# Performance work log

Hardware: AMD Instinct MI355X
Metric: run time of the kernel (lower is better)

## Reference

```python
import jax, jax.numpy as jnp
import numpy as np

DIM = 1024
H = 8            # heads (light and heavy)
DH = 64          # dim_head
W = 64           # local attention window (light_window_size // 2)
NQ = 512         # num_heavy_tokens_q
NKV = 1024       # num_heavy_tokens_kv
EPS = 1.0        # coor descent eps
NITERS = 50      # coor descent iters
FETCH = 9.0 / 8.0
SCALE = DH ** -0.5


def _ln(x, w, b):
    m = x.mean(-1, keepdims=True)
    v = ((x - m) ** 2).mean(-1, keepdims=True)
    return (x - m) * jax.lax.rsqrt(v + 1e-5) * w + b


def _rms(x, g):
    n = jnp.maximum(jnp.linalg.norm(x, axis=-1, keepdims=True), 1e-12)
    return x / n * np.sqrt(DIM).astype(np.float32) * g


def local_attn(x, Wqkv, Wout):
    # LocalMHA, non-causal, look_backward=1, look_forward=1, window W
    b, n, _ = x.shape
    nw = n // W
    qkv = x @ Wqkv.T                      # [b,n,3*H*DH]
    q, k, v = jnp.split(qkv, 3, axis=-1)
    def towin(t):
        return t.reshape(b, nw, W, H, DH).transpose(0, 3, 1, 2, 4)  # [b,h,nw,w,dh]
    q, k, v = map(towin, (q, k, v))
    def expand(t):  # gather prev/cur/next windows -> [b,h,nw,3w,dh]
        tp = jnp.pad(t, ((0, 0), (0, 0), (1, 1), (0, 0), (0, 0)))
        return jnp.concatenate([tp[:, :, :-2], tp[:, :, 1:-1], tp[:, :, 2:]], axis=3)
    ke, ve = expand(k), expand(v)
    sim = jnp.einsum('bhnid,bhnjd->bhnij', q, ke) * SCALE
    win = jnp.arange(nw)
    valid = jnp.concatenate([
        jnp.repeat((win > 0)[:, None], W, 1),
        jnp.ones((nw, W), bool),
        jnp.repeat((win < nw - 1)[:, None], W, 1)], axis=1)  # [nw,3w]
    sim = jnp.where(valid[None, None, :, None, :], sim, -1e9)
    attn = jax.nn.softmax(sim, axis=-1)
    o = jnp.einsum('bhnij,bhnjd->bhnid', attn, ve)
    o = o.transpose(0, 2, 3, 1, 4).reshape(b, n, H * DH)
    return o @ Wout.T


def route(x, routing_token, num_tokens):
    # CoordinateDescentRouter with num_routing_tokens=1, straight_through=True
    s = jnp.einsum('bnd,rd->brn', x, routing_token).reshape(x.shape[0], x.shape[1])
    n = s.shape[-1]
    logk = jnp.log(jnp.asarray(min(num_tokens * FETCH, float(n)), s.dtype))
    def body(ab, _):
        a, bb = ab
        a = EPS * (logk - jax.nn.logsumexp((s + bb) / EPS, axis=-1, keepdims=True))
        bb = -jax.nn.relu(s + a)
        return (a, bb), None
    (a, bb), _ = jax.lax.scan(body, (jnp.zeros((s.shape[0], 1), s.dtype), -s), None, length=NITERS)
    scores = jnp.exp((s + a + bb) / EPS)
    sel_scores, sel_idx = jax.lax.top_k(scores, num_tokens)
    # straight-through: forward value 1.0, gradient of identity
    sel_scores = sel_scores + jax.lax.stop_gradient(1.0 - sel_scores)
    return sel_scores, sel_idx


def heavy_attn(xq, ctx, scores_kv, gamma, Wq, Wkv, Wout, null_kv):
    b = xq.shape[0]
    xq = _rms(xq, gamma)
    ctx = _rms(ctx, gamma)
    q = (xq @ Wq.T).reshape(b, -1, H, DH).transpose(0, 2, 1, 3)           # [b,h,nq,dh]
    kv = (ctx @ Wkv.T).reshape(b, -1, H, 2 * DH).transpose(0, 2, 1, 3)    # [b,h,nkv,2dh]
    k, v = kv[..., :DH], kv[..., DH:]
    v = v * scores_kv[:, None, :, None]
    nk = jnp.broadcast_to(null_kv[0][None, :, None, :], (b, H, 1, DH))
    nv = jnp.broadcast_to(null_kv[1][None, :, None, :], (b, H, 1, DH))
    k = jnp.concatenate([nk, k], axis=2)
    v = jnp.concatenate([nv, v], axis=2)
    sim = jnp.einsum('bhid,bhjd->bhij', q, k) * SCALE
    attn = jax.nn.softmax(sim, axis=-1)
    o = jnp.einsum('bhij,bhjd->bhid', attn, v)
    o = o.transpose(0, 2, 1, 3).reshape(b, -1, H * DH)
    return o @ Wout.T


def setup_inputs() -> dict:
    key = jax.random.key(0)
    ks = jax.random.split(key, 12)
    D, IN = DIM, H * DH
    w = lambda k, shape: jax.random.normal(k, shape, jnp.float32) * 0.02
    return {
        'x': jax.random.normal(ks[0], (4, 4096, D), jnp.float32),
        'ln_w': jnp.ones((D,), jnp.float32),
        'ln_b': jnp.zeros((D,), jnp.float32),
        'Wqkv': w(ks[1], (3 * IN, D)),
        'Wout_l': w(ks[2], (D, IN)),
        'rt_q': jax.random.normal(ks[3], (1, D), jnp.float32),
        'rt_kv': jax.random.normal(ks[4], (1, D), jnp.float32),
        'gamma': jnp.ones((D,), jnp.float32),
        'Wq': w(ks[5], (IN, D)),
        'Wkv': w(ks[6], (2 * IN, D)),
        'Wout_h': w(ks[7], (D, IN)),
        'null_kv': jax.random.normal(ks[8], (2, H, DH), jnp.float32),
        'null_q': jax.random.normal(ks[9], (D,), jnp.float32),
    }


def reference(x, ln_w, ln_b, Wqkv, Wout_l, rt_q, rt_kv, gamma, Wq, Wkv, Wout_h, null_kv, null_q):
    b, n, d = x.shape
    light = local_attn(_ln(x, ln_w, ln_b), Wqkv, Wout_l)
    sq, iq = route(x, rt_q, NQ)
    skv, ikv = route(x, rt_kv, NKV)
    br = jnp.arange(b)[:, None]
    xq = x[br, iq]          # gather routed queries  [b,NQ,d]
    xkv = x[br, ikv]        # gather routed kv       [b,NKV,d]
    heavy = heavy_attn(xq, xkv, skv, gamma, Wq, Wkv, Wout_h, null_kv)
    heavy = heavy * sq[..., None]
    out = jnp.broadcast_to(null_q[None, None, :], (b, n, d))
    out = out.at[br, iq].set(heavy)   # scatter heavy branch back
    return out + light
```

## Files before the change

kernel.cpp:

```cpp
#include <hip/hip_runtime.h>
#include <hip/hip_bf16.h>

typedef __attribute__((ext_vector_type(8))) short bv8;
typedef __attribute__((ext_vector_type(4))) float fv4;
typedef __hip_bfloat16 bf16;

#define MFMA16(a,b,c) __builtin_amdgcn_mfma_f32_16x16x32_bf16((a),(b),(c),0,0,0)
#define GLOAD_LDS(gp, lp) __builtin_amdgcn_global_load_lds( \
    (const __attribute__((address_space(1))) void*)(gp), \
    (__attribute__((address_space(3))) void*)(lp), 16, 0, 0)

template<int NW>
__device__ __forceinline__ float blockReduceSumF(float v) {
  #pragma unroll
  for (int m = 1; m < 64; m <<= 1) v += __shfl_xor(v, m, 64);
  __shared__ float sm[NW];
  if ((threadIdx.x & 63) == 0) sm[threadIdx.x >> 6] = v;
  __syncthreads();
  float t = 0.f;
  #pragma unroll
  for (int i = 0; i < NW; ++i) t += sm[i];
  __syncthreads();
  return t;
}

template<int NW>
__device__ __forceinline__ double blockReduceMaxD(double v) {
  #pragma unroll
  for (int m = 1; m < 64; m <<= 1) v = fmax(v, __shfl_xor(v, m, 64));
  __shared__ double sm[NW];
  if ((threadIdx.x & 63) == 0) sm[threadIdx.x >> 6] = v;
  __syncthreads();
  double t = sm[0];
  #pragma unroll
  for (int i = 1; i < NW; ++i) t = fmax(t, sm[i]);
  __syncthreads();
  return t;
}

__global__ __launch_bounds__(256)
void prep_kernel(const float* __restrict__ x, const float* __restrict__ lnw,
                 const float* __restrict__ lnb, const float* __restrict__ rtq,
                 const float* __restrict__ rtkv, bf16* __restrict__ lnout,
                 double* __restrict__ s,
                 const float* __restrict__ a0, const float* __restrict__ a1,
                 const float* __restrict__ a2, const float* __restrict__ a3,
                 const float* __restrict__ a4,
                 bf16* __restrict__ b0, bf16* __restrict__ b1, bf16* __restrict__ b2,
                 bf16* __restrict__ b3, bf16* __restrict__ b4,
                 int* __restrict__ posq) {
  const int bid = blockIdx.x;
  if (bid < 16384) {
    const int r = bid;
    const float* xr = x + (size_t)r * 1024;
    float v4[4]; float ssum = 0.f;
    double dq = 0.0, dk = 0.0;
    #pragma unroll
    for (int i = 0; i < 4; ++i) {
      int d = threadIdx.x + i * 256;
      float v = xr[d];
      v4[i] = v; ssum += v;
      dq += (double)v * (double)rtq[d];
      dk += (double)v * (double)rtkv[d];
    }
    ssum = blockReduceSumF<4>(ssum);
    const float mean = ssum * (1.0f / 1024.0f);
    float vs = 0.f;
    #pragma unroll
    for (int i = 0; i < 4; ++i) { float d = v4[i] - mean; vs += d * d; }
    vs = blockReduceSumF<4>(vs);
    const float rstd = 1.0f / sqrtf(vs * (1.0f / 1024.0f) + 1e-5f);
    #pragma unroll
    for (int m = 1; m < 64; m <<= 1) { dq += __shfl_xor(dq, m, 64); dk += __shfl_xor(dk, m, 64); }
    __shared__ double smq[4], smk[4];
    if ((threadIdx.x & 63) == 0) { smq[threadIdx.x >> 6] = dq; smk[threadIdx.x >> 6] = dk; }
    __syncthreads();
    if (threadIdx.x == 0) {
      s[r] = smq[0] + smq[1] + smq[2] + smq[3];
      s[16384 + r] = smk[0] + smk[1] + smk[2] + smk[3];
    }
    bf16* orow = lnout + (size_t)r * 1024;
    #pragma unroll
    for (int i = 0; i < 4; ++i) {
      int d = threadIdx.x + i * 256;
      orow[d] = __float2bfloat16((v4[i] - mean) * rstd * lnw[d] + lnb[d]);
    }
  } else if (bid < 18432) {
    size_t g = ((size_t)(bid - 16384) * 256 + threadIdx.x) * 8;
    const float* src; bf16* dst; size_t off;
    if (g < 1572864)      { src = a0; dst = b0; off = g; }
    else if (g < 2097152) { src = a1; dst = b1; off = g - 1572864; }
    else if (g < 2621440) { src = a2; dst = b2; off = g - 2097152; }
    else if (g < 3670016) { src = a3; dst = b3; off = g - 2621440; }
    else                  { src = a4; dst = b4; off = g - 3670016; }
    float4 v0 = *(const float4*)(src + off);
    float4 v1 = *(const float4*)(src + off + 4);
    bv8 o;
    ((bf16*)&o)[0] = __float2bfloat16(v0.x); ((bf16*)&o)[1] = __float2bfloat16(v0.y);
    ((bf16*)&o)[2] = __float2bfloat16(v0.z); ((bf16*)&o)[3] = __float2bfloat16(v0.w);
    ((bf16*)&o)[4] = __float2bfloat16(v1.x); ((bf16*)&o)[5] = __float2bfloat16(v1.y);
    ((bf16*)&o)[6] = __float2bfloat16(v1.z); ((bf16*)&o)[7] = __float2bfloat16(v1.w);
    *(bv8*)(dst + off) = o;
  } else {
    int i0 = (bid - 18432) * 1024 + threadIdx.x * 4;
    posq[i0] = -1; posq[i0 + 1] = -1; posq[i0 + 2] = -1; posq[i0 + 3] = -1;
  }
}

template<int EPI>
__device__ __forceinline__ void gemm_core(
    const bf16* __restrict__ A, const bf16* __restrict__ B, void* __restrict__ Cout,
    int N, int K, int row0, int col0, bf16* As, bf16* Bs,
    const int* __restrict__ posq, const float* __restrict__ heavy,
    const float* __restrict__ nullq) {
  const int tid = threadIdx.x;
  const int lane = tid & 63, w = tid >> 6;
  const int wr = w >> 1, wc = w & 1;
  const int lrow = lane & 15, lkg = lane >> 4;
  fv4 acc[4][4];
  #pragma unroll
  for (int m = 0; m < 4; ++m)
    #pragma unroll
    for (int n = 0; n < 4; ++n) acc[m][n] = (fv4){0.f, 0.f, 0.f, 0.f};
  const int ob0 = w * 1024;
  for (int k0 = 0; k0 < K; k0 += 64) {
    #pragma unroll
    for (int t = 0; t < 4; ++t) {
      int ob = t * 4096 + ob0;
      int byteL = ob + lane * 16;
      int r = byteL >> 7;
      int cU = ((byteL >> 4) & 7) ^ (r & 7);
      GLOAD_LDS(A + (size_t)(row0 + r) * K + k0 + cU * 8, (char*)As + ob);
      GLOAD_LDS(B + (size_t)(col0 + r) * K + k0 + cU * 8, (char*)Bs + ob);
    }
    __syncthreads();
    #pragma unroll
    for (int ks = 0; ks < 2; ++ks) {
      bv8 af[4], bfr[4];
      #pragma unroll
      for (int m = 0; m < 4; ++m) {
        int row = wr * 64 + m * 16 + lrow;
        af[m] = *(bv8*)((char*)As + row * 128 + (((ks * 4 + lkg) ^ (row & 7)) << 4));
      }
      #pragma unroll
      for (int n = 0; n < 4; ++n) {
        int row = wc * 64 + n * 16 + lrow;
        bfr[n] = *(bv8*)((char*)Bs + row * 128 + (((ks * 4 + lkg) ^ (row & 7)) << 4));
      }
      #pragma unroll
      for (int m = 0; m < 4; ++m)
        #pragma unroll
        for (int n = 0; n < 4; ++n)
          acc[m][n] = MFMA16(af[m], bfr[n], acc[m][n]);
    }
    __syncthreads();
  }
  #pragma unroll
  for (int m = 0; m < 4; ++m) {
    int gr0 = row0 + wr * 64 + m * 16 + (lane >> 4) * 4;
    #pragma unroll
    for (int n = 0; n < 4; ++n) {
      int gc = col0 + wc * 64 + n * 16 + lrow;
      #pragma unroll
      for (int r = 0; r < 4; ++r) {
        int grow = gr0 + r;
        float vv = acc[m][n][r];
        if (EPI == 0) {
          ((bf16*)Cout)[(size_t)grow * N + gc] = __float2bfloat16(vv);
        } else if (EPI == 1) {
          ((float*)Cout)[(size_t)grow * N + gc] = vv;
        } else {
          int p = posq[grow];
          float add = (p >= 0) ? heavy[((size_t)((grow >> 12) * 512 + p)) * 1024 + gc]
                               : nullq[gc];
          ((float*)Cout)[(size_t)grow * N + gc] = vv + add;
        }
      }
    }
  }
}

__device__ __forceinline__ void xcd_remap(int d, int gx, int& row0, int& col0) {
  int q = d >> 3;
  col0 = (q % gx) * 128;
  row0 = ((d & 7) + 8 * (q / gx)) * 128;
}

template<int EPI>
__global__ __launch_bounds__(256)
void gemm_bt(const bf16* __restrict__ A, const bf16* __restrict__ B, void* __restrict__ Cout,
             int N, int K,
             const int* __restrict__ posq, const float* __restrict__ heavy,
             const float* __restrict__ nullq) {
  __shared__ alignas(16) bf16 As[128 * 64];
  __shared__ alignas(16) bf16 Bs[128 * 64];
  int row0, col0;
  xcd_remap(blockIdx.y * gridDim.x + blockIdx.x, gridDim.x, row0, col0);
  gemm_core<EPI>(A, B, Cout, N, K, row0, col0, As, Bs, posq, heavy, nullq);
}

__global__ __launch_bounds__(256)
void qkv_route_kernel(const bf16* __restrict__ ln, const bf16* __restrict__ Wqkv,
                      bf16* __restrict__ qkv,
                      const double* __restrict__ s_all, int* __restrict__ iq,
                      int* __restrict__ ikv, int* __restrict__ posq) {
  __shared__ __align__(16) char arena[34816];
  const int bid = blockIdx.x;
  const int tid = threadIdx.x;
  if (bid >= 8) {
    bf16* As = (bf16*)arena;
    bf16* Bs = (bf16*)(arena + 16384);
    int row0, col0;
    xcd_remap(bid - 8, 12, row0, col0);
    gemm_core<0>(ln, Wqkv, qkv, 1536, 1024, row0, col0, As, Bs, nullptr, nullptr, nullptr);
  } else {
    const int route = bid >> 2, b = bid & 3;
    const double* s = s_all + route * 16384 + b * 4096;
    const double Kk = (route == 0) ? 576.0 : 1152.0;
    const int KSEL = (route == 0) ? 512 : 1024;
    const int lane = tid & 63, wid = tid >> 6;
    unsigned long long* keys = (unsigned long long*)arena;
    int* scn = (int*)(arena + 32768);
    double* red = (double*)(arena + 33792);
    double sv[16];
    #pragma unroll
    for (int i = 0; i < 16; ++i) sv[i] = s[tid * 16 + i];
    double mx = sv[0];
    #pragma unroll
    for (int i = 1; i < 16; ++i) mx = fmax(mx, sv[i]);
    mx = blockReduceMaxD<4>(mx);
    double ev[16];
    #pragma unroll
    for (int i = 0; i < 16; ++i) ev[i] = exp(sv[i] - mx);
    double z = (4096.0 / Kk) * exp(-mx);
    for (int it = 1; it < 50; ++it) {
      double t0 = 0.0, t1 = 0.0;
      #pragma unroll
      for (int i = 0; i < 16; i += 2) { t0 += fmin(ev[i], z); t1 += fmin(ev[i + 1], z); }
      double t = t0 + t1;
      #pragma unroll
      for (int m = 1; m < 64; m <<= 1) t += __shfl_xor(t, m, 64);
      if (lane == 0) red[wid] = t;
      __syncthreads();
      z = (red[0] + red[1] + red[2] + red[3]) / Kk;
      __syncthreads();
    }
    const double a = -mx - log(z);
    float scf[16]; int m16 = 0;
    #pragma unroll
    for (int i = 0; i < 16; ++i) {
      scf[i] = (float)exp(fmin(sv[i] + a, 0.0));
      m16 += (scf[i] == 1.0f) ? 1 : 0;
    }
    scn[tid] = m16;
    __syncthreads();
    for (int off = 1; off < 256; off <<= 1) {
      int v = (tid >= off) ? scn[tid - off] : 0;
      __syncthreads();
      scn[tid] += v;
      __syncthreads();
    }
    const int total = scn[255];
    const int excl = scn[tid] - m16;
    if (total >= KSEL) {
      int rk = excl;
      #pragma unroll
      for (int i = 0; i < 16; ++i) {
        if (scf[i] == 1.0f) {
          if (rk < KSEL) {
            int idx = tid * 16 + i;
            if (route == 0) { iq[b * 512 + rk] = idx; posq[b * 4096 + idx] = rk; }
            else            { ikv[b * 1024 + rk] = idx; }
          }
          rk++;
        }
      }
    } else {
      #pragma unroll
      for (int i = 0; i < 16; ++i) {
        unsigned bits = __float_as_uint(scf[i]);
        keys[tid * 16 + i] = ((unsigned long long)(~bits) << 32) | (unsigned long long)(tid * 16 + i);
      }
      for (int k = 2; k <= 4096; k <<= 1) {
        for (int j = k >> 1; j > 0; j >>= 1) {
          __syncthreads();
          for (int t = tid; t < 2048; t += 256) {
            int i2 = ((t & ~(j - 1)) << 1) | (t & (j - 1));
            int ip = i2 + j;
            unsigned long long av = keys[i2], bvv = keys[ip];
            bool up = ((i2 & k) == 0);
            if (up ? (av > bvv) : (av < bvv)) { keys[i2] = bvv; keys[ip] = av; }
          }
        }
      }
      __syncthreads();
      for (int j2 = tid; j2 < KSEL; j2 += 256) {
        int idx = (int)(keys[j2] & 0xFFFFFFFFull);
        if (route == 0) { iq[b * 512 + j2] = idx; posq[b * 4096 + idx] = j2; }
        else            { ikv[b * 1024 + j2] = idx; }
      }
    }
  }
}

__global__ __launch_bounds__(256)
void la_gather_kernel(const bf16* __restrict__ qkv, bf16* __restrict__ olight,
                      const float* __restrict__ x, const float* __restrict__ gamma,
                      const int* __restrict__ iq, const int* __restrict__ ikv,
                      bf16* __restrict__ xq, bf16* __restrict__ xkv) {
  __shared__ bf16 Qs[64][72], Ks[64][72], Vts[64][72], Ps[64][72];
  const int tid = threadIdx.x;
  if (blockIdx.x < 2048) {
    const int w = blockIdx.x & 63, h = (blockIdx.x >> 6) & 7, b = blockIdx.x >> 9;
    const int lane = tid & 63, wv = tid >> 6;
    const int lrow = lane & 15, lkg = lane >> 4;
    {
      const size_t baseq = ((size_t)(b * 4096 + w * 64)) * 1536 + h * 64;
      #pragma unroll
      for (int v = 0; v < 2; ++v) {
        int vec = tid + v * 256; int i = vec >> 3, dd = (vec & 7) * 8;
        *(bv8*)&Qs[i][dd] = *(const bv8*)&qkv[baseq + (size_t)i * 1536 + dd];
      }
    }
    fv4 oacc[4];
    float m_run[4], l_run[4];
    #pragma unroll
    for (int n = 0; n < 4; ++n) oacc[n] = (fv4){0.f, 0.f, 0.f, 0.f};
    #pragma unroll
    for (int r = 0; r < 4; ++r) { m_run[r] = -INFINITY; l_run[r] = 0.f; }
    for (int c = 0; c < 3; ++c) {
      int sw = w - 1 + c;
      if (sw < 0 || sw >= 64) continue;
      __syncthreads();
      const size_t bkv = ((size_t)(b * 4096 + sw * 64)) * 1536 + h * 64;
      #pragma unroll
      for (int v = 0; v < 2; ++v) {
        int vec = tid + v * 256; int i = vec >> 3, dd = (vec & 7) * 8;
        *(bv8*)&Ks[i][dd] = *(const bv8*)&qkv[bkv + 512 + (size_t)i * 1536 + dd];
      }
      #pragma unroll
      for (int v = 0; v < 2; ++v) {
        int vec = tid + v * 256; int j = vec >> 3, d0 = (vec & 7) * 8;
        bv8 val = *(const bv8*)&qkv[bkv + 1024 + (size_t)j * 1536 + d0];
        #pragma unroll
        for (int i = 0; i < 8; ++i) Vts[d0 + i][j] = ((bf16*)&val)[i];
      }
      __syncthreads();
      fv4 sa[4];
      #pragma unroll
      for (int n = 0; n < 4; ++n) {
        sa[n] = (fv4){0.f, 0.f, 0.f, 0.f};
        #pragma unroll
        for (int ks = 0; ks < 2; ++ks) {
          bv8 aq = *(bv8*)&Qs[wv * 16 + lrow][lkg * 8 + ks * 32];
          bv8 bk = *(bv8*)&Ks[n * 16 + lrow][lkg * 8 + ks * 32];
          sa[n] = MFMA16(aq, bk, sa[n]);
        }
      }
      float mc[4];
      #pragma unroll
      for (int r = 0; r < 4; ++r) {
        #pragma unroll
        for (int n = 0; n < 4; ++n) sa[n][r] *= 0.125f;
        mc[r] = fmaxf(fmaxf(sa[0][r], sa[1][r]), fmaxf(sa[2][r], sa[3][r]));
      }
      #pragma unroll
      for (int m = 1; m < 16; m <<= 1)
        #pragma unroll
        for (int r = 0; r < 4; ++r) mc[r] = fmaxf(mc[r], __shfl_xor(mc[r], m, 64));
      float p[4][4], ls[4];
      #pragma unroll
      for (int r = 0; r < 4; ++r) {
        float mn = fmaxf(m_run[r], mc[r]);
        float scl = expf(m_run[r] - mn);
        ls[r] = 0.f;
        #pragma unroll
        for (int n = 0; n < 4; ++n) { p[n][r] = expf(sa[n][r] - mn); ls[r] += p[n][r]; }
        m_run[r] = mn;
        l_run[r] *= scl;
        #pragma unroll
        for (int n = 0; n < 4; ++n) oacc[n][r] *= scl;
      }
      #pragma unroll
      for (int m = 1; m < 16; m <<= 1)
        #pragma unroll
        for (int r = 0; r < 4; ++r) ls[r] += __shfl_xor(ls[r], m, 64);
      #pragma unroll
      for (int r = 0; r < 4; ++r) l_run[r] += ls[r];
      #pragma unroll
      for (int n = 0; n < 4; ++n)
        #pragma unroll
        for (int r = 0; r < 4; ++r)
          Ps[wv * 16 + lkg * 4 + r][n * 16 + lrow] = __float2bfloat16(p[n][r]);
      __syncthreads();
      #pragma unroll
      for (int n = 0; n < 4; ++n)
        #pragma unroll
        for (int ks = 0; ks < 2; ++ks) {
          bv8 ap = *(bv8*)&Ps[wv * 16 + lrow][lkg * 8 + ks * 32];
          bv8 bvv = *(bv8*)&Vts[n * 16 + lrow][lkg * 8 + ks * 32];
          oacc[n] = MFMA16(ap, bvv, oacc[n]);
        }
    }
    const size_t ob = ((size_t)(b * 4096 + w * 64 + wv * 16)) * 512 + h * 64;
    #pragma unroll
    for (int n = 0; n < 4; ++n)
      #pragma unroll
      for (int r = 0; r < 4; ++r) {
        int row = lkg * 4 + r;
        olight[ob + (size_t)row * 512 + n * 16 + lrow] = __float2bfloat16(oacc[n][r] / l_run[r]);
      }
  } else {
    const int gid = blockIdx.x - 2048;
    const float* src; bf16* dst;
    if (gid < 2048) {
      int b = gid >> 9, j = gid & 511;
      int tok = iq[b * 512 + j];
      src = x + ((size_t)(b * 4096 + tok)) * 1024;
      dst = xq + (size_t)gid * 1024;
    } else {
      int id = gid - 2048;
      int b = id >> 10, j = id & 1023;
      int tok = ikv[b * 1024 + j];
      src = x + ((size_t)(b * 4096 + tok)) * 1024;
      dst = xkv + (size_t)id * 1024;
    }
    float v4[4]; float ss = 0.f;
    #pragma unroll
    for (int i = 0; i < 4; ++i) { v4[i] = src[tid + i * 256]; ss += v4[i] * v4[i]; }
    ss = blockReduceSumF<4>(ss);
    const float nrm = fmaxf(sqrtf(ss), 1e-12f);
    const float scl = 32.0f / nrm;
    #pragma unroll
    for (int i = 0; i < 4; ++i) {
      int d = tid + i * 256;
      dst[d] = __float2bfloat16(v4[i] * scl * gamma[d]);
    }
  }
}

__global__ __launch_bounds__(256)
void wqkv_kernel(const bf16* __restrict__ xkv, const bf16* __restrict__ Wkv,
                 bf16* __restrict__ kvh,
                 const bf16* __restrict__ xq, const bf16* __restrict__ Wq,
                 bf16* __restrict__ qh) {
  __shared__ alignas(16) bf16 As[128 * 64];
  __shared__ alignas(16) bf16 Bs[128 * 64];
  const int bid = blockIdx.x;
  int row0, col0;
  if (bid < 256) {
    xcd_remap(bid, 8, row0, col0);
    gemm_core<0>(xkv, Wkv, kvh, 1024, 1024, row0, col0, As, Bs, nullptr, nullptr, nullptr);
  } else {
    xcd_remap(bid - 256, 4, row0, col0);
    gemm_core<0>(xq, Wq, qh, 512, 1024, row0, col0, As, Bs, nullptr, nullptr, nullptr);
  }
}

__global__ __launch_bounds__(256)
void heavy_attn_split_kernel(const bf16* __restrict__ qh, const bf16* __restrict__ kvh,
                             const float* __restrict__ nkv, bf16* __restrict__ o_part,
                             float* __restrict__ ml_part) {
  const int qt = blockIdx.x, h = blockIdx.y;
  const int b = blockIdx.z >> 2, s = blockIdx.z & 3;
  const int tid = threadIdx.x;
  const int lane = tid & 63, wv = tid >> 6;
  const int lrow = lane & 15, lkg = lane >> 4;
  __shared__ bf16 Qs[64][72], Ks[64][72], Vts[64][72], Ps[64][72];
  {
    const size_t baseq = ((size_t)(b * 512 + qt * 64)) * 512 + h * 64;
    #pragma unroll
    for (int v = 0; v < 2; ++v) {
      int vec = tid + v * 256; int i = vec >> 3, dd = (vec & 7) * 8;
      *(bv8*)&Qs[i][dd] = *(const bv8*)&qh[baseq + (size_t)i * 512 + dd];
    }
  }
  fv4 oacc[4];
  float m_run[4], l_run[4];
  #pragma unroll
  for (int n = 0; n < 4; ++n) oacc[n] = (fv4){0.f, 0.f, 0.f, 0.f};
  #pragma unroll
  for (int r = 0; r < 4; ++r) { m_run[r] = -INFINITY; l_run[r] = 0.f; }
  const int cs = (s == 0) ? 0 : (s * 4 + 1);
  const int ce = s * 4 + 5;
  for (int c = cs; c < ce; ++c) {
    __syncthreads();
    #pragma unroll
    for (int v = 0; v < 2; ++v) {
      int vec = tid + v * 256; int j = vec >> 3, dd = (vec & 7) * 8;
      int kvg = c * 64 + j;
      bv8 val;
      if (kvg >= 1 && kvg <= 1024) {
        val = *(const bv8*)&kvh[((size_t)(b * 1024 + kvg - 1)) * 1024 + h * 128 + dd];
      } else if (kvg == 0) {
        #pragma unroll
        for (int t = 0; t < 8; ++t) ((bf16*)&val)[t] = __float2bfloat16(nkv[h * 64 + dd + t]);
      } else {
        #pragma unroll
        for (int t = 0; t < 8; ++t) ((short*)&val)[t] = 0;
      }
      *(bv8*)&Ks[j][dd] = val;
    }
    #pragma unroll
    for (int v = 0; v < 2; ++v) {
      int vec = tid + v * 256; int j = vec >> 3, d0 = (vec & 7) * 8;
      int kvg = c * 64 + j;
      if (kvg >= 1 && kvg <= 1024) {
        bv8 val = *(const bv8*)&kvh[((size_t)(b * 1024 + kvg - 1)) * 1024 + h * 128 + 64 + d0];
        #pragma unroll
        for (int i = 0; i < 8; ++i) Vts[d0 + i][j] = ((bf16*)&val)[i];
      } else if (kvg == 0) {
        #pragma unroll
        for (int i = 0; i < 8; ++i) Vts[d0 + i][j] = __float2bfloat16(nkv[512 + h * 64 + d0 + i]);
      } else {
        #pragma unroll
        for (int i = 0; i < 8; ++i) Vts[d0 + i][j] = __float2bfloat16(0.0f);
      }
    }
    __syncthreads();
    fv4 sa[4];
    #pragma unroll
    for (int n = 0; n < 4; ++n) {
      sa[n] = (fv4){0.f, 0.f, 0.f, 0.f};
      #pragma unroll
      for (int ks = 0; ks < 2; ++ks) {
        bv8 aq = *(bv8*)&Qs[wv * 16 + lrow][lkg * 8 + ks * 32];
        bv8 bk = *(bv8*)&Ks[n * 16 + lrow][lkg * 8 + ks * 32];
        sa[n] = MFMA16(aq, bk, sa[n]);
      }
    }
    float mc[4];
    #pragma unroll
    for (int r = 0; r < 4; ++r) {
      #pragma unroll
      for (int n = 0; n < 4; ++n) {
        sa[n][r] *= 0.125f;
        int kvg = c * 64 + n * 16 + lrow;
        if (kvg > 1024) sa[n][r] = -1e30f;
      }
      mc[r] = fmaxf(fmaxf(sa[0][r], sa[1][r]), fmaxf(sa[2][r], sa[3][r]));
    }
    #pragma unroll
    for (int m = 1; m < 16; m <<= 1)
      #pragma unroll
      for (int r = 0; r < 4; ++r) mc[r] = fmaxf(mc[r], __shfl_xor(mc[r], m, 64));
    float p[4][4], ls[4];
    #pragma unroll
    for (int r = 0; r < 4; ++r) {
      float mn = fmaxf(m_run[r], mc[r]);
      float scl = expf(m_run[r] - mn);
      ls[r] = 0.f;
      #pragma unroll
      for (int n = 0; n < 4; ++n) { p[n][r] = expf(sa[n][r] - mn); ls[r] += p[n][r]; }
      m_run[r] = mn;
      l_run[r] *= scl;
      #pragma unroll
      for (int n = 0; n < 4; ++n) oacc[n][r] *= scl;
    }
    #pragma unroll
    for (int m = 1; m < 16; m <<= 1)
      #pragma unroll
      for (int r = 0; r < 4; ++r) ls[r] += __shfl_xor(ls[r], m, 64);
    #pragma unroll
    for (int r = 0; r < 4; ++r) l_run[r] += ls[r];
    #pragma unroll
    for (int n = 0; n < 4; ++n)
      #pragma unroll
      for (int r = 0; r < 4; ++r)
        Ps[wv * 16 + lkg * 4 + r][n * 16 + lrow] = __float2bfloat16(p[n][r]);
    __syncthreads();
    #pragma unroll
    for (int n = 0; n < 4; ++n)
      #pragma unroll
      for (int ks = 0; ks < 2; ++ks) {
        bv8 ap = *(bv8*)&Ps[wv * 16 + lrow][lkg * 8 + ks * 32];
        bv8 bvv = *(bv8*)&Vts[n * 16 + lrow][lkg * 8 + ks * 32];
        oacc[n] = MFMA16(ap, bvv, oacc[n]);
      }
  }
  const int idx = (((s * 4 + b) * 8 + h) * 8 + qt);
  bf16* ob = o_part + (size_t)idx * 4096;
  #pragma unroll
  for (int n = 0; n < 4; ++n)
    #pragma unroll
    for (int r = 0; r < 4; ++r) {
      int row = wv * 16 + lkg * 4 + r;
      ob[row * 64 + n * 16 + lrow] = __float2bfloat16(oacc[n][r]);
    }
  if (lrow == 0) {
    #pragma unroll
    for (int r = 0; r < 4; ++r) {
      int row = wv * 16 + lkg * 4 + r;
      ml_part[idx * 128 + row] = m_run[r];
      ml_part[idx * 128 + 64 + row] = l_run[r];
    }
  }
}

__global__ __launch_bounds__(256)
void wouth_gemm_kernel(const bf16* __restrict__ o_part, const float* __restrict__ ml_part,
                       const bf16* __restrict__ B, float* __restrict__ Cout) {
  __shared__ alignas(16) bf16 As[128 * 32];
  __shared__ alignas(16) bf16 Bs[128 * 32];
  const int N = 1024, K = 512;
  int row0, col0;
  xcd_remap(blockIdx.y * gridDim.x + blockIdx.x, gridDim.x, row0, col0);
  const int tid = threadIdx.x;
  const int lane = tid & 63, w = tid >> 6;
  const int wr = w >> 1, wc = w & 1;
  const int lrow = lane & 15, lk = (lane >> 4) * 8;
  fv4 acc[4][4];
  #pragma unroll
  for (int m = 0; m < 4; ++m)
    #pragma unroll
    for (int n = 0; n < 4; ++n) acc[m][n] = (fv4){0.f, 0.f, 0.f, 0.f};
  const int ob0 = w * 2048;
  for (int k0 = 0; k0 < K; k0 += 32) {
    #pragma unroll
    for (int t = 0; t < 2; ++t) {
      int ob = ob0 + t * 1024;
      int ofl = ob + lane * 16;
      int r = ofl >> 6, c8 = ((ofl >> 4) & 3) * 8;
      int grow = row0 + r, k = k0 + c8;
      int b = grow >> 9, qrow = grow & 511;
      int qt = qrow >> 6, row_in = qrow & 63;
      int h = k >> 6, d0 = k & 63;
      bv8 v[4]; float m[4], l[4];
      #pragma unroll
      for (int s = 0; s < 4; ++s) {
        int idx = (((s * 4 + b) * 8 + h) * 8 + qt);
        v[s] = *(const bv8*)&o_part[(size_t)idx * 4096 + row_in * 64 + d0];
        m[s] = ml_part[idx * 128 + row_in];
        l[s] = ml_part[idx * 128 + 64 + row_in];
      }
      float mstar = fmaxf(fmaxf(m[0], m[1]), fmaxf(m[2], m[3]));
      float ws[4]; float wsum = 0.f;
      #pragma unroll
      for (int s = 0; s < 4; ++s) { ws[s] = expf(m[s] - mstar); wsum += ws[s] * l[s]; }
      const float inv = 1.0f / wsum;
      bv8 o8;
      #pragma unroll
      for (int j = 0; j < 8; ++j) {
        float acc8 = 0.f;
        #pragma unroll
        for (int s = 0; s < 4; ++s) acc8 += ws[s] * __bfloat162float(((bf16*)&v[s])[j]);
        ((bf16*)&o8)[j] = __float2bfloat16(acc8 * inv);
      }
      *(bv8*)((char*)As + ofl) = o8;
      GLOAD_LDS(B + (size_t)(col0 + r) * K + k0 + c8, (char*)Bs + ob);
    }
    __syncthreads();
    bv8 af[4], bfr[4];
    #pragma unroll
    for (int m2 = 0; m2 < 4; ++m2) af[m2] = *(bv8*)&As[(wr * 64 + m2 * 16 + lrow) * 32 + lk];
    #pragma unroll
    for (int n = 0; n < 4; ++n) bfr[n] = *(bv8*)&Bs[(wc * 64 + n * 16 + lrow) * 32 + lk];
    #pragma unroll
    for (int m2 = 0; m2 < 4; ++m2)
      #pragma unroll
      for (int n = 0; n < 4; ++n)
        acc[m2][n] = MFMA16(af[m2], bfr[n], acc[m2][n]);
    __syncthreads();
  }
  #pragma unroll
  for (int m2 = 0; m2 < 4; ++m2) {
    int gr0 = row0 + wr * 64 + m2 * 16 + (lane >> 4) * 4;
    #pragma unroll
    for (int n = 0; n < 4; ++n) {
      int gc = col0 + wc * 64 + n * 16 + lrow;
      #pragma unroll
      for (int r = 0; r < 4; ++r)
        Cout[(size_t)(gr0 + r) * N + gc] = acc[m2][n][r];
    }
  }
}

extern "C" void kernel_launch(void* const* d_in, const int* in_sizes, int n_in,
                              void* d_out, int out_size, void* d_ws, size_t ws_size,
                              hipStream_t stream) {
  (void)in_sizes; (void)n_in; (void)out_size; (void)ws_size;
  const float* x     = (const float*)d_in[0];
  const float* ln_w  = (const float*)d_in[1];
  const float* ln_b  = (const float*)d_in[2];
  const float* Wqkv  = (const float*)d_in[3];
  const float* Woutl = (const float*)d_in[4];
  const float* rtq   = (const float*)d_in[5];
  const float* rtkv  = (const float*)d_in[6];
  const float* gamma = (const float*)d_in[7];
  const float* Wq    = (const float*)d_in[8];
  const float* Wkv   = (const float*)d_in[9];
  const float* Wouth = (const float*)d_in[10];
  const float* nkv   = (const float*)d_in[11];
  const float* nq    = (const float*)d_in[12];
  float* out = (float*)d_out;

  char* ws = (char*)d_ws;
  size_t off = 0;
  auto alloc = [&](size_t bytes) -> void* {
    void* p = ws + off;
    off = (off + bytes + 255) & ~(size_t)255;
    return p;
  };
  bf16* ln_bf    = (bf16*)alloc(16384ull * 1024 * 2);
  bf16* qkv_bf   = (bf16*)alloc(16384ull * 1536 * 2);
  bf16* ol_bf    = (bf16*)alloc(16384ull * 512 * 2);
  bf16* Wqkv_bf  = (bf16*)alloc(1536ull * 1024 * 2);
  bf16* Woutl_bf = (bf16*)alloc(1024ull * 512 * 2);
  bf16* Wq_bf    = (bf16*)alloc(512ull * 1024 * 2);
  bf16* Wkv_bf   = (bf16*)alloc(1024ull * 1024 * 2);
  bf16* Wouth_bf = (bf16*)alloc(1024ull * 512 * 2);
  double* s_d    = (double*)alloc(32768ull * 8);
  int* iq        = (int*)alloc(2048ull * 4);
  int* ikv       = (int*)alloc(4096ull * 4);
  int* posq      = (int*)alloc(16384ull * 4);
  bf16* xq_bf    = (bf16*)alloc(2048ull * 1024 * 2);
  bf16* xkv_bf   = (bf16*)alloc(4096ull * 1024 * 2);
  bf16* qh_bf    = (bf16*)alloc(2048ull * 512 * 2);
  bf16* kvh_bf   = (bf16*)alloc(4096ull * 1024 * 2);
  float* heavy_f = (float*)alloc(2048ull * 1024 * 4);
  bf16* o_part   = (bf16*)alloc(4096ull * 4096 * 2);
  float* ml_part = (float*)alloc(4096ull * 128 * 4);

  prep_kernel<<<18448, 256, 0, stream>>>(x, ln_w, ln_b, rtq, rtkv, ln_bf, s_d,
                                         Wqkv, Woutl, Wq, Wkv, Wouth,
                                         Wqkv_bf, Woutl_bf, Wq_bf, Wkv_bf, Wouth_bf,
                                         posq);

  qkv_route_kernel<<<1544, 256, 0, stream>>>(ln_bf, Wqkv_bf, qkv_bf,
                                             s_d, iq, ikv, posq);

  la_gather_kernel<<<8192, 256, 0, stream>>>(qkv_bf, ol_bf, x, gamma, iq, ikv, xq_bf, xkv_bf);

  wqkv_kernel<<<320, 256, 0, stream>>>(xkv_bf, Wkv_bf, kvh_bf, xq_bf, Wq_bf, qh_bf);

  heavy_attn_split_kernel<<<dim3(8, 8, 16), 256, 0, stream>>>(qh_bf, kvh_bf, nkv, o_part, ml_part);

  wouth_gemm_kernel<<<dim3(8, 16), 256, 0, stream>>>(o_part, ml_part, Wouth_bf, heavy_f);

  gemm_bt<2><<<dim3(8, 128), 256, 0, stream>>>(ol_bf, Woutl_bf, out, 1024, 512,
                                               posq, heavy_f, nq);
}
```

Baseline: 273.1 us.

## Fuse light output GEMM into Wq/Wkv launch and scatter heavy output in-place

Moves the light-attention output projection into the same launch as the heavy Q/KV projections, so those independent GEMMs share one grid. The heavy output projection now adds its result directly into the final output rows selected by iq, which removes the heavy_f buffer and its gather in the final epilogue. The shared GEMM core drops from K-tile 64 with an XOR-swizzled LDS layout to K-tile 32 with an unswizzled layout. This shrinks LDS use but risks bank conflicts and doubles the number of barriers. The sort keys move from LDS to a global workspace, and the in-place add depends on iq holding no duplicate rows.

```diff
diff --git a/kernel.cpp b/kernel.cpp
--- a/kernel.cpp
+++ b/kernel.cpp
@@ -111,48 +111,37 @@
 __device__ __forceinline__ void gemm_core(
     const bf16* __restrict__ A, const bf16* __restrict__ B, void* __restrict__ Cout,
     int N, int K, int row0, int col0, bf16* As, bf16* Bs,
-    const int* __restrict__ posq, const float* __restrict__ heavy,
-    const float* __restrict__ nullq) {
+    const int* __restrict__ posq, const float* __restrict__ nullq) {
   const int tid = threadIdx.x;
   const int lane = tid & 63, w = tid >> 6;
   const int wr = w >> 1, wc = w & 1;
-  const int lrow = lane & 15, lkg = lane >> 4;
+  const int lrow = lane & 15, lk = (lane >> 4) * 8;
   fv4 acc[4][4];
   #pragma unroll
   for (int m = 0; m < 4; ++m)
     #pragma unroll
     for (int n = 0; n < 4; ++n) acc[m][n] = (fv4){0.f, 0.f, 0.f, 0.f};
-  const int ob0 = w * 1024;
-  for (int k0 = 0; k0 < K; k0 += 64) {
-    #pragma unroll
-    for (int t = 0; t < 4; ++t) {
-      int ob = t * 4096 + ob0;
-      int byteL = ob + lane * 16;
-      int r = byteL >> 7;
-      int cU = ((byteL >> 4) & 7) ^ (r & 7);
-      GLOAD_LDS(A + (size_t)(row0 + r) * K + k0 + cU * 8, (char*)As + ob);
-      GLOAD_LDS(B + (size_t)(col0 + r) * K + k0 + cU * 8, (char*)Bs + ob);
-    }
-    __syncthreads();
-    #pragma unroll
-    for (int ks = 0; ks < 2; ++ks) {
-      bv8 af[4], bfr[4];
-      #pragma unroll
-      for (int m = 0; m < 4; ++m) {
-        int row = wr * 64 + m * 16 + lrow;
-        af[m] = *(bv8*)((char*)As + row * 128 + (((ks * 4 + lkg) ^ (row & 7)) << 4));
-      }
-      #pragma unroll
-      for (int n = 0; n < 4; ++n) {
-        int row = wc * 64 + n * 16 + lrow;
-        bfr[n] = *(bv8*)((char*)Bs + row * 128 + (((ks * 4 + lkg) ^ (row & 7)) << 4));
-      }
-      #pragma unroll
-      for (int m = 0; m < 4; ++m)
-        #pragma unroll
-        for (int n = 0; n < 4; ++n)
-          acc[m][n] = MFMA16(af[m], bfr[n], acc[m][n]);
-    }
+  const int ob0 = w * 2048;
+  for (int k0 = 0; k0 < K; k0 += 32) {
+    #pragma unroll
+    for (int t = 0; t < 2; ++t) {
+      int ob = ob0 + t * 1024;
+      int ofl = ob + lane * 16;
+      int r = ofl >> 6, c8 = ((ofl >> 4) & 3) * 8;
+      GLOAD_LDS(A + (size_t)(row0 + r) * K + k0 + c8, (char*)As + ob);
+      GLOAD_LDS(B + (size_t)(col0 + r) * K + k0 + c8, (char*)Bs + ob);
+    }
+    __syncthreads();
+    bv8 af[4], bfr[4];
+    #pragma unroll
+    for (int m = 0; m < 4; ++m) af[m] = *(bv8*)&As[(wr * 64 + m * 16 + lrow) * 32 + lk];
+    #pragma unroll
+    for (int n = 0; n < 4; ++n) bfr[n] = *(bv8*)&Bs[(wc * 64 + n * 16 + lrow) * 32 + lk];
+    #pragma unroll
+    for (int m = 0; m < 4; ++m)
+      #pragma unroll
+      for (int n = 0; n < 4; ++n)
+        acc[m][n] = MFMA16(af[m], bfr[n], acc[m][n]);
     __syncthreads();
   }
   #pragma unroll
@@ -167,12 +156,8 @@
         float vv = acc[m][n][r];
         if (EPI == 0) {
           ((bf16*)Cout)[(size_t)grow * N + gc] = __float2bfloat16(vv);
-        } else if (EPI == 1) {
-          ((float*)Cout)[(size_t)grow * N + gc] = vv;
         } else {
-          int p = posq[grow];
-          float add = (p >= 0) ? heavy[((size_t)((grow >> 12) * 512 + p)) * 1024 + gc]
-                               : nullq[gc];
+          float add = (posq[grow] >= 0) ? 0.0f : nullq[gc];
           ((float*)Cout)[(size_t)grow * N + gc] = vv + add;
         }
       }
@@ -186,42 +171,28 @@
   row0 = ((d & 7) + 8 * (q / gx)) * 128;
 }
 
-template<int EPI>
-__global__ __launch_bounds__(256)
-void gemm_bt(const bf16* __restrict__ A, const bf16* __restrict__ B, void* __restrict__ Cout,
-             int N, int K,
-             const int* __restrict__ posq, const float* __restrict__ heavy,
-             const float* __restrict__ nullq) {
-  __shared__ alignas(16) bf16 As[128 * 64];
-  __shared__ alignas(16) bf16 Bs[128 * 64];
-  int row0, col0;
-  xcd_remap(blockIdx.y * gridDim.x + blockIdx.x, gridDim.x, row0, col0);
-  gemm_core<EPI>(A, B, Cout, N, K, row0, col0, As, Bs, posq, heavy, nullq);
-}
-
 __global__ __launch_bounds__(256)
 void qkv_route_kernel(const bf16* __restrict__ ln, const bf16* __restrict__ Wqkv,
                       bf16* __restrict__ qkv,
                       const double* __restrict__ s_all, int* __restrict__ iq,
-                      int* __restrict__ ikv, int* __restrict__ posq) {
-  __shared__ __align__(16) char arena[34816];
+                      int* __restrict__ ikv, int* __restrict__ posq,
+                      unsigned long long* __restrict__ keys_ws) {
+  __shared__ alignas(16) bf16 As[128 * 32];
+  __shared__ alignas(16) bf16 Bs[128 * 32];
+  __shared__ int scn[256];
+  __shared__ double red[4];
   const int bid = blockIdx.x;
   const int tid = threadIdx.x;
   if (bid >= 8) {
-    bf16* As = (bf16*)arena;
-    bf16* Bs = (bf16*)(arena + 16384);
     int row0, col0;
     xcd_remap(bid - 8, 12, row0, col0);
-    gemm_core<0>(ln, Wqkv, qkv, 1536, 1024, row0, col0, As, Bs, nullptr, nullptr, nullptr);
+    gemm_core<0>(ln, Wqkv, qkv, 1536, 1024, row0, col0, As, Bs, nullptr, nullptr);
   } else {
     const int route = bid >> 2, b = bid & 3;
     const double* s = s_all + route * 16384 + b * 4096;
     const double Kk = (route == 0) ? 576.0 : 1152.0;
     const int KSEL = (route == 0) ? 512 : 1024;
     const int lane = tid & 63, wid = tid >> 6;
-    unsigned long long* keys = (unsigned long long*)arena;
-    int* scn = (int*)(arena + 32768);
-    double* red = (double*)(arena + 33792);
     double sv[16];
     #pragma unroll
     for (int i = 0; i < 16; ++i) sv[i] = s[tid * 16 + i];
@@ -276,6 +247,7 @@
         }
       }
     } else {
+      unsigned long long* keys = keys_ws + (size_t)bid * 4096;
       #pragma unroll
       for (int i = 0; i < 16; ++i) {
         unsigned bits = __float_as_uint(scf[i]);
@@ -440,20 +412,26 @@
 }
 
 __global__ __launch_bounds__(256)
-void wqkv_kernel(const bf16* __restrict__ xkv, const bf16* __restrict__ Wkv,
-                 bf16* __restrict__ kvh,
-                 const bf16* __restrict__ xq, const bf16* __restrict__ Wq,
-                 bf16* __restrict__ qh) {
-  __shared__ alignas(16) bf16 As[128 * 64];
-  __shared__ alignas(16) bf16 Bs[128 * 64];
+void lightout_wqkv_kernel(const bf16* __restrict__ ol, const bf16* __restrict__ Woutl,
+                          float* __restrict__ out,
+                          const int* __restrict__ posq, const float* __restrict__ nq,
+                          const bf16* __restrict__ xkv, const bf16* __restrict__ Wkv,
+                          bf16* __restrict__ kvh,
+                          const bf16* __restrict__ xq, const bf16* __restrict__ Wq,
+                          bf16* __restrict__ qh) {
+  __shared__ alignas(16) bf16 As[128 * 32];
+  __shared__ alignas(16) bf16 Bs[128 * 32];
   const int bid = blockIdx.x;
   int row0, col0;
   if (bid < 256) {
     xcd_remap(bid, 8, row0, col0);
-    gemm_core<0>(xkv, Wkv, kvh, 1024, 1024, row0, col0, As, Bs, nullptr, nullptr, nullptr);
+    gemm_core<0>(xkv, Wkv, kvh, 1024, 1024, row0, col0, As, Bs, nullptr, nullptr);
+  } else if (bid < 320) {
+    xcd_remap(bid - 256, 4, row0, col0);
+    gemm_core<0>(xq, Wq, qh, 512, 1024, row0, col0, As, Bs, nullptr, nullptr);
   } else {
-    xcd_remap(bid - 256, 4, row0, col0);
-    gemm_core<0>(xq, Wq, qh, 512, 1024, row0, col0, As, Bs, nullptr, nullptr, nullptr);
+    xcd_remap(bid - 320, 8, row0, col0);
+    gemm_core<2>(ol, Woutl, out, 1024, 512, row0, col0, As, Bs, posq, nq);
   }
 }
 
@@ -598,8 +576,9 @@
 }
 
 __global__ __launch_bounds__(256)
-void wouth_gemm_kernel(const bf16* __restrict__ o_part, const float* __restrict__ ml_part,
-                       const bf16* __restrict__ B, float* __restrict__ Cout) {
+void wouth_scatter_kernel(const bf16* __restrict__ o_part, const float* __restrict__ ml_part,
+                          const bf16* __restrict__ B, float* __restrict__ out,
+                          const int* __restrict__ iq) {
   __shared__ alignas(16) bf16 As[128 * 32];
   __shared__ alignas(16) bf16 Bs[128 * 32];
   const int N = 1024, K = 512;
@@ -669,8 +648,13 @@
     for (int n = 0; n < 4; ++n) {
       int gc = col0 + wc * 64 + n * 16 + lrow;
       #pragma unroll
-      for (int r = 0; r < 4; ++r)
-        Cout[(size_t)(gr0 + r) * N + gc] = acc[m2][n][r];
+      for (int r = 0; r < 4; ++r) {
+        int grow = gr0 + r;
+        int b = grow >> 9;
+        int tok = iq[grow];
+        float* op = out + ((size_t)(b * 4096 + tok)) * 1024 + gc;
+        *op += acc[m2][n][r];
+      }
     }
   }
 }
@@ -717,9 +701,9 @@
   bf16* xkv_bf   = (bf16*)alloc(4096ull * 1024 * 2);
   bf16* qh_bf    = (bf16*)alloc(2048ull * 512 * 2);
   bf16* kvh_bf   = (bf16*)alloc(4096ull * 1024 * 2);
-  float* heavy_f = (float*)alloc(2048ull * 1024 * 4);
   bf16* o_part   = (bf16*)alloc(4096ull * 4096 * 2);
   float* ml_part = (float*)alloc(4096ull * 128 * 4);
+  unsigned long long* keys_ws = (unsigned long long*)alloc(8ull * 4096 * 8);
 
   prep_kernel<<<18448, 256, 0, stream>>>(x, ln_w, ln_b, rtq, rtkv, ln_bf, s_d,
                                          Wqkv, Woutl, Wq, Wkv, Wouth,
@@ -727,16 +711,15 @@
                                          posq);
 
   qkv_route_kernel<<<1544, 256, 0, stream>>>(ln_bf, Wqkv_bf, qkv_bf,
-                                             s_d, iq, ikv, posq);
+                                             s_d, iq, ikv, posq, keys_ws);
 
   la_gather_kernel<<<8192, 256, 0, stream>>>(qkv_bf, ol_bf, x, gamma, iq, ikv, xq_bf, xkv_bf);
 
-  wqkv_kernel<<<320, 256, 0, stream>>>(xkv_bf, Wkv_bf, kvh_bf, xq_bf, Wq_bf, qh_bf);
+  lightout_wqkv_kernel<<<1344, 256, 0, stream>>>(ol_bf, Woutl_bf, out, posq, nq,
+                                                 xkv_bf, Wkv_bf, kvh_bf,
+                                                 xq_bf, Wq_bf, qh_bf);
 
   heavy_attn_split_kernel<<<dim3(8, 8, 16), 256, 0, stream>>>(qh_bf, kvh_bf, nkv, o_part, ml_part);
 
-  wouth_gemm_kernel<<<dim3(8, 16), 256, 0, stream>>>(o_part, ml_part, Wouth_bf, heavy_f);
-
-  gemm_bt<2><<<dim3(8, 128), 256, 0, stream>>>(ol_bf, Woutl_bf, out, 1024, 512,
-                                               posq, heavy_f, nq);
-}
+  wouth_scatter_kernel<<<dim3(8, 16), 256, 0, stream>>>(o_part, ml_part, Wouth_bf, out, iq);
+}
```

After: 299.7 us. 1.1x slower.
